# Performance work log

Measured on AMD Instinct MI355X. Metric: run time of the kernel, lower is better.

The kernel has to match this reference:

```python
import jax, jax.numpy as jnp
import numpy as np

EPS = 1e-7  # K.epsilon()


def setup_inputs() -> dict:
    key = jax.random.key(0)
    k1, k2, k3, k4 = jax.random.split(key, 4)
    B, T, S = 512, 32, 2048  # batch, time_steps, seq_len
    inputs = jax.random.normal(k1, (B, T, S), dtype=jnp.float32)
    # Keras mask (float 0/1), same shape as inputs
    mask = (jax.random.uniform(k2, (B, T, S)) < 0.8).astype(jnp.float32)
    # 'uniform' keras initializer: U(-0.05, 0.05)
    W = jax.random.uniform(k3, (S, T, T), minval=-0.05, maxval=0.05, dtype=jnp.float32)
    b = jax.random.uniform(k4, (S, T), minval=-0.05, maxval=0.05, dtype=jnp.float32)
    return {"inputs": inputs, "mask": mask, "W": W, "b": b}


def reference(inputs, mask, W, b):
    # (B,T,S) -> (B,S,T), apply mask
    x = jnp.transpose(inputs, (0, 2, 1)) * jnp.transpose(mask, (0, 2, 1))
    # per-position matmul, batched over B and S (replaces the tf.scan over batch)
    z = jnp.einsum('bst,stu->bsu', x, W) + b  # (B,S,T)
    e = jnp.exp(jnp.tanh(z))
    att = e / (jnp.sum(e, axis=2, keepdims=True) + EPS)  # softmax-like over T
    return jnp.sum(att * x, axis=1)  # (B,T)
```

## Files before the change

### kernel.cpp

```cpp
#include <hip/hip_runtime.h>

#define EPS_K 1e-7f

typedef __attribute__((ext_vector_type(8)))  short          frag8;
typedef __attribute__((ext_vector_type(16))) float          accf16;
typedef __attribute__((ext_vector_type(4)))  unsigned short us4;
typedef __attribute__((ext_vector_type(4)))  float          f32x4;

__device__ __forceinline__ unsigned f2bf(float f) {
  union { float f; unsigned u; } v; v.f = f;
  unsigned u = v.u;
  u += 0x7FFFu + ((u >> 16) & 1u);
  return u >> 16;
}
__device__ __forceinline__ float bf2f(unsigned short s) {
  union { unsigned u; float f; } v; v.u = ((unsigned)s) << 16;
  return v.f;
}
__device__ __forceinline__ unsigned pk_bf16(float lo, float hi) {
  return f2bf(lo) | (f2bf(hi) << 16);
}
__device__ __forceinline__ float rcp_f(float x) {
  return __builtin_amdgcn_rcpf(x);
}

__global__ __launch_bounds__(256) void wbf_prep(
    const float* __restrict__ Wt, unsigned short* __restrict__ Wbf)
{
  __shared__ unsigned short tile[32 * 33];
  const int s   = blockIdx.x;
  const int tid = threadIdx.x;
  {
    const int t  = tid >> 3;
    const int uc = tid & 7;
    const float4 v = *(const float4*)(Wt + s * 1024 + t * 32 + 4 * uc);
    tile[t * 33 + 4 * uc + 0] = (unsigned short)f2bf(v.x);
    tile[t * 33 + 4 * uc + 1] = (unsigned short)f2bf(v.y);
    tile[t * 33 + 4 * uc + 2] = (unsigned short)f2bf(v.z);
    tile[t * 33 + 4 * uc + 3] = (unsigned short)f2bf(v.w);
  }
  __syncthreads();
  {
    const int u  = tid >> 3;
    const int tc = tid & 7;
    uint2 d;
    d.x = (unsigned)tile[(4 * tc + 0) * 33 + u] | ((unsigned)tile[(4 * tc + 1) * 33 + u] << 16);
    d.y = (unsigned)tile[(4 * tc + 2) * 33 + u] | ((unsigned)tile[(4 * tc + 3) * 33 + u] << 16);
    *(uint2*)(Wbf + s * 1024 + u * 32 + 4 * tc) = d;
  }
}

__global__ __launch_bounds__(512, 2) void repack(
    const float* __restrict__ inp, const float* __restrict__ msk,
    unsigned short* __restrict__ Y)
{
  __shared__ unsigned short sl[32768];
  const int tid  = threadIdx.x;
  const int lane = tid & 63;
  const int b7   = tid >> 6;
  const int Q    = blockIdx.x & 63;
  const int w    = blockIdx.x >> 6;
  const int l31  = lane & 31;
  const int l5   = lane >> 5;

  const size_t rb = ((size_t)(Q * 8 + b7) * 32 + 8 * l5) * 2048 + w * 128 + 4 * l31;
  const int slot = b7 ^ (l31 & 7);

  #pragma unroll 1
  for (int c2 = 0; c2 < 2; ++c2) {
    f32x4 vi[8], vm[8];
    #pragma unroll
    for (int j = 0; j < 8; ++j) {
      const size_t off = rb + (size_t)(16 * c2 + j) * 2048;
      vi[j] = *(const f32x4*)(inp + off);
      vm[j] = *(const f32x4*)(msk + off);
    }
    const int c   = 2 * c2 + l5;
    const int sid = c * 8 + slot;
    #pragma unroll
    for (int k = 0; k < 4; ++k) {
      const int s_loc = 4 * l31 + k;
      uint4 d;
      d.x = pk_bf16(vi[0][k] * vm[0][k], vi[1][k] * vm[1][k]);
      d.y = pk_bf16(vi[2][k] * vm[2][k], vi[3][k] * vm[3][k]);
      d.z = pk_bf16(vi[4][k] * vm[4][k], vi[5][k] * vm[5][k]);
      d.w = pk_bf16(vi[6][k] * vm[6][k], vi[7][k] * vm[7][k]);
      *(uint4*)(sl + s_loc * 256 + ((sid ^ (s_loc & 7)) * 8)) = d;
    }
  }
  __syncthreads();

  const size_t ybyte = ((size_t)Q * 2048 + (size_t)w * 128) * 512;
  #pragma unroll
  for (int i = 0; i < 8; ++i) {
    const int e  = i * 512 + tid;
    const int sv = e >> 5, ch = e & 31;
    const uint4 d = *(const uint4*)(sl + sv * 256 + ((ch ^ (sv & 7)) * 8));
    *(uint4*)((char*)Y + ybyte + (size_t)e * 16) = d;
  }
}

__global__ __launch_bounds__(256, 4) void attn_comp(
    const unsigned short* __restrict__ Y,
    const unsigned short* __restrict__ Wbf,
    const float* __restrict__ bias,
    float* __restrict__ part)
{
  __shared__ float red[4096];
  const int tid  = threadIdx.x;
  const int bg   = blockIdx.x & 15;
  const int sg   = blockIdx.x >> 4;
  const int lane = tid & 63;
  const int wv   = tid >> 6;
  const int n    = lane & 31;
  const int h    = lane >> 5;

  const unsigned short* Yq = Y + ((size_t)(bg * 4 + (n >> 3)) * 2048) * 256;

  float O[16];
  #pragma unroll
  for (int r = 0; r < 16; ++r) O[r] = 0.f;

  #pragma unroll 2
  for (int it = 0; it < 8; ++it) {
    const int s = sg * 32 + wv * 8 + it;
    const unsigned short* slp = Yq + (size_t)s * 256;
    const int bt = (((n & 7) ^ ((s >> 2) & 7)) * 8);

    const frag8 b1 = *(const frag8*)(slp + h * 64 + bt);
    const frag8 b2 = *(const frag8*)(slp + (h + 2) * 64 + bt);

    const unsigned short* wp = Wbf + (size_t)s * 1024 + n * 32 + 8 * h;
    const frag8 a1 = *(const frag8*)(wp);
    const frag8 a2 = *(const frag8*)(wp + 16);

    accf16 acc;
    #pragma unroll
    for (int g = 0; g < 4; ++g) {
      const f32x4 bb = *(const f32x4*)(bias + s * 32 + 8 * g + 4 * h);
      acc[4 * g + 0] = bb[0]; acc[4 * g + 1] = bb[1];
      acc[4 * g + 2] = bb[2]; acc[4 * g + 3] = bb[3];
    }
    acc = __builtin_amdgcn_mfma_f32_32x32x16_bf16(a1, b1, acc, 0, 0, 0);
    acc = __builtin_amdgcn_mfma_f32_32x32x16_bf16(a2, b2, acc, 0, 0, 0);

    float ps = 0.f;
    #pragma unroll
    for (int r = 0; r < 16; ++r) {
      const float z  = acc[r];
      const float e2 = __expf(2.f * z);
      const float th = 1.f - 2.f * rcp_f(e2 + 1.f);
      acc[r] = __expf(th);
      ps    += acc[r];
    }
    const float tot = ps + __shfl_xor(ps, 32, 64);
    const float inv = rcp_f(tot + EPS_K);

    #pragma unroll
    for (int g = 0; g < 4; ++g) {
      const us4 xv = *(const us4*)(slp + g * 64 + bt + 4 * h);
      #pragma unroll
      for (int i = 0; i < 4; ++i)
        O[4 * g + i] += acc[4 * g + i] * inv * bf2f(xv[i]);
    }
  }

  #pragma unroll
  for (int r = 0; r < 16; ++r) {
    const int u = (r & 3) + 8 * (r >> 2) + 4 * h;
    red[wv * 1024 + n * 32 + (u ^ n)] = O[r];
  }
  __syncthreads();

  const int q0 = tid * 4;
  f32x4 v;
  #pragma unroll
  for (int i = 0; i < 4; ++i) {
    const int q = q0 + i;
    const int b = q >> 5, u = q & 31;
    float sum = 0.f;
    #pragma unroll
    for (int w = 0; w < 4; ++w) sum += red[w * 1024 + b * 32 + (u ^ b)];
    v[i] = sum;
  }
  *(f32x4*)(part + (size_t)sg * 16384 + bg * 1024 + q0) = v;
}

__global__ __launch_bounds__(256) void reduce_part(
    const float* __restrict__ part, float* __restrict__ out)
{
  const int f = blockIdx.x * 256 + threadIdx.x;
  float s = 0.f;
  #pragma unroll 8
  for (int sg = 0; sg < 64; ++sg) s += part[(size_t)sg * 16384 + f];
  out[f] = s;
}

__global__ __launch_bounds__(256) void attn_naive(
    const float* __restrict__ inp, const float* __restrict__ msk,
    const float* __restrict__ Wt, const float* __restrict__ bias,
    float* __restrict__ out)
{
  const int idx = blockIdx.x * 256 + threadIdx.x;
  const int b = idx >> 5, sc = idx & 31;
  float O[32];
  #pragma unroll
  for (int u = 0; u < 32; ++u) O[u] = 0.f;
  for (int si = 0; si < 64; ++si) {
    const int s = sc * 64 + si;
    float x[32], z[32];
    for (int t = 0; t < 32; ++t) {
      x[t] = inp[((size_t)b * 32 + t) * 2048 + s] * msk[((size_t)b * 32 + t) * 2048 + s];
      z[t] = bias[s * 32 + t];
    }
    for (int t = 0; t < 32; ++t) {
      const float xv = x[t];
      for (int u = 0; u < 32; ++u) z[u] += xv * Wt[(size_t)s * 1024 + t * 32 + u];
    }
    float e[32], ps = 0.f;
    for (int u = 0; u < 32; ++u) { e[u] = expf(tanhf(z[u])); ps += e[u]; }
    const float inv = 1.f / (ps + EPS_K);
    for (int u = 0; u < 32; ++u) O[u] += e[u] * inv * x[u];
  }
  for (int u = 0; u < 32; ++u) atomicAdd(out + b * 32 + u, O[u]);
}

extern "C" void kernel_launch(void* const* d_in, const int* in_sizes, int n_in,
                              void* d_out, int out_size, void* d_ws, size_t ws_size,
                              hipStream_t stream) {
  const float* inp  = (const float*)d_in[0];
  const float* msk  = (const float*)d_in[1];
  const float* Wt   = (const float*)d_in[2];
  const float* bias = (const float*)d_in[3];
  float* out = (float*)d_out;

  const size_t part_sz = (size_t)64 * 16384 * sizeof(float);
  const size_t wbf_sz  = (size_t)2048 * 1024 * sizeof(unsigned short);
  const size_t y_sz    = (size_t)512 * 32 * 2048 * sizeof(unsigned short);

  if (ws_size >= part_sz + wbf_sz + y_sz) {
    float* part = (float*)d_ws;
    unsigned short* Wbf = (unsigned short*)((char*)d_ws + part_sz);
    unsigned short* Y   = (unsigned short*)((char*)d_ws + part_sz + wbf_sz);
    repack<<<dim3(1024), dim3(512), 0, stream>>>(inp, msk, Y);
    wbf_prep<<<dim3(2048), dim3(256), 0, stream>>>(Wt, Wbf);
    attn_comp<<<dim3(1024), dim3(256), 0, stream>>>(Y, Wbf, bias, part);
    reduce_part<<<dim3(64), dim3(256), 0, stream>>>(part, out);
  } else {
    (void)hipMemsetAsync(out, 0, (size_t)out_size * sizeof(float), stream);
    attn_naive<<<dim3(64), dim3(256), 0, stream>>>(inp, msk, Wt, bias, out);
  }
}
```

Measured before the change: 347.8 us.

## Fuse masking and bf16 repack into attention kernel, dropping intermediate Y buffer

Removes the separate repack kernel that wrote a bf16 copy of the masked inputs to global memory. The attention kernel now loads inputs and mask with nontemporal loads, packs them into an LDS tile, and runs 16x16x32 MFMAs directly from shared memory. This saves a full write and re-read of the intermediate tensor and one launch, and halves the partial-sum buffer. In exchange each block needs 64KB of LDS, which limits occupancy, and the reads are exposed with no separate staging pass to hide them.

```diff
diff --git a/kernel.cpp b/kernel.cpp
--- a/kernel.cpp
+++ b/kernel.cpp
@@ -3,7 +3,7 @@
 #define EPS_K 1e-7f
 
 typedef __attribute__((ext_vector_type(8)))  short          frag8;
-typedef __attribute__((ext_vector_type(16))) float          accf16;
+typedef __attribute__((ext_vector_type(4)))  float          accf4;
 typedef __attribute__((ext_vector_type(4)))  unsigned short us4;
 typedef __attribute__((ext_vector_type(4)))  float          f32x4;
 
@@ -20,8 +20,8 @@
 __device__ __forceinline__ unsigned pk_bf16(float lo, float hi) {
   return f2bf(lo) | (f2bf(hi) << 16);
 }
-__device__ __forceinline__ float rcp_f(float x) {
-  return __builtin_amdgcn_rcpf(x);
+__device__ __forceinline__ f32x4 ld_nt(const float* p) {
+  return __builtin_nontemporal_load((const f32x4*)p);
 }
 
 __global__ __launch_bounds__(256) void wbf_prep(
@@ -50,140 +50,124 @@
   }
 }
 
-__global__ __launch_bounds__(512, 2) void repack(
-    const float* __restrict__ inp, const float* __restrict__ msk,
-    unsigned short* __restrict__ Y)
-{
-  __shared__ unsigned short sl[32768];
-  const int tid  = threadIdx.x;
-  const int lane = tid & 63;
-  const int b7   = tid >> 6;
-  const int Q    = blockIdx.x & 63;
-  const int w    = blockIdx.x >> 6;
-  const int l31  = lane & 31;
-  const int l5   = lane >> 5;
-
-  const size_t rb = ((size_t)(Q * 8 + b7) * 32 + 8 * l5) * 2048 + w * 128 + 4 * l31;
-  const int slot = b7 ^ (l31 & 7);
-
-  #pragma unroll 1
-  for (int c2 = 0; c2 < 2; ++c2) {
-    f32x4 vi[8], vm[8];
-    #pragma unroll
-    for (int j = 0; j < 8; ++j) {
-      const size_t off = rb + (size_t)(16 * c2 + j) * 2048;
-      vi[j] = *(const f32x4*)(inp + off);
-      vm[j] = *(const f32x4*)(msk + off);
-    }
-    const int c   = 2 * c2 + l5;
-    const int sid = c * 8 + slot;
-    #pragma unroll
-    for (int k = 0; k < 4; ++k) {
-      const int s_loc = 4 * l31 + k;
-      uint4 d;
-      d.x = pk_bf16(vi[0][k] * vm[0][k], vi[1][k] * vm[1][k]);
-      d.y = pk_bf16(vi[2][k] * vm[2][k], vi[3][k] * vm[3][k]);
-      d.z = pk_bf16(vi[4][k] * vm[4][k], vi[5][k] * vm[5][k]);
-      d.w = pk_bf16(vi[6][k] * vm[6][k], vi[7][k] * vm[7][k]);
-      *(uint4*)(sl + s_loc * 256 + ((sid ^ (s_loc & 7)) * 8)) = d;
-    }
-  }
-  __syncthreads();
-
-  const size_t ybyte = ((size_t)Q * 2048 + (size_t)w * 128) * 512;
-  #pragma unroll
-  for (int i = 0; i < 8; ++i) {
-    const int e  = i * 512 + tid;
-    const int sv = e >> 5, ch = e & 31;
-    const uint4 d = *(const uint4*)(sl + sv * 256 + ((ch ^ (sv & 7)) * 8));
-    *(uint4*)((char*)Y + ybyte + (size_t)e * 16) = d;
-  }
-}
-
-__global__ __launch_bounds__(256, 4) void attn_comp(
-    const unsigned short* __restrict__ Y,
+template <bool USE_WS>
+__global__ __launch_bounds__(512, 4) void attn_fused(
+    const float* __restrict__ inp,
+    const float* __restrict__ msk,
     const unsigned short* __restrict__ Wbf,
     const float* __restrict__ bias,
-    float* __restrict__ part)
-{
-  __shared__ float red[4096];
-  const int tid  = threadIdx.x;
-  const int bg   = blockIdx.x & 15;
-  const int sg   = blockIdx.x >> 4;
+    float* __restrict__ part,
+    float* __restrict__ out)
+{
+  __shared__ unsigned short x_us[16 * 2048];
+
+  const int tid = threadIdx.x;
+  const int st  = blockIdx.x & 31;
+  const int bg  = blockIdx.x >> 5;
+  const int s0  = st * 64;
+
+  const int sc = tid & 15;
+  const int bl = (tid >> 4) & 3;
+  const int hi = tid >> 6;
+  const int b_s = (hi & 3) * 4 + bl;
+  #pragma unroll
+  for (int it = 0; it < 2; ++it) {
+    const int tb = (hi >> 2) | (it << 1);
+    const float* ip = inp + ((size_t)(bg * 16 + b_s) * 32 + 8 * tb) * 2048 + s0 + 4 * sc;
+    const float* mp = msk + ((size_t)(bg * 16 + b_s) * 32 + 8 * tb) * 2048 + s0 + 4 * sc;
+    f32x4 vi[8], vm[8];
+    #pragma unroll
+    for (int r = 0; r < 8; ++r) {
+      vi[r] = ld_nt(ip + r * 2048);
+      vm[r] = ld_nt(mp + r * 2048);
+    }
+    #pragma unroll
+    for (int w = 0; w < 4; ++w) {
+      const int L = tb * 64 + 4 * sc + w;
+      uint4 d;
+      d.x = pk_bf16(vi[0][w] * vm[0][w], vi[1][w] * vm[1][w]);
+      d.y = pk_bf16(vi[2][w] * vm[2][w], vi[3][w] * vm[3][w]);
+      d.z = pk_bf16(vi[4][w] * vm[4][w], vi[5][w] * vm[5][w]);
+      d.w = pk_bf16(vi[6][w] * vm[6][w], vi[7][w] * vm[7][w]);
+      *(uint4*)(x_us + b_s * 2048 + ((L ^ (b_s & 7)) * 8)) = d;
+    }
+  }
+  __syncthreads();
+
   const int lane = tid & 63;
   const int wv   = tid >> 6;
-  const int n    = lane & 31;
-  const int h    = lane >> 5;
-
-  const unsigned short* Yq = Y + ((size_t)(bg * 4 + (n >> 3)) * 2048) * 256;
-
-  float O[16];
-  #pragma unroll
-  for (int r = 0; r < 16; ++r) O[r] = 0.f;
-
-  #pragma unroll 2
-  for (int it = 0; it < 8; ++it) {
-    const int s = sg * 32 + wv * 8 + it;
-    const unsigned short* slp = Yq + (size_t)s * 256;
-    const int bt = (((n & 7) ^ ((s >> 2) & 7)) * 8);
-
-    const frag8 b1 = *(const frag8*)(slp + h * 64 + bt);
-    const frag8 b2 = *(const frag8*)(slp + (h + 2) * 64 + bt);
-
-    const unsigned short* wp = Wbf + (size_t)s * 1024 + n * 32 + 8 * h;
-    const frag8 a1 = *(const frag8*)(wp);
-    const frag8 a2 = *(const frag8*)(wp + 16);
-
-    accf16 acc;
-    #pragma unroll
-    for (int g = 0; g < 4; ++g) {
-      const f32x4 bb = *(const f32x4*)(bias + s * 32 + 8 * g + 4 * h);
-      acc[4 * g + 0] = bb[0]; acc[4 * g + 1] = bb[1];
-      acc[4 * g + 2] = bb[2]; acc[4 * g + 3] = bb[3];
-    }
-    acc = __builtin_amdgcn_mfma_f32_32x32x16_bf16(a1, b1, acc, 0, 0, 0);
-    acc = __builtin_amdgcn_mfma_f32_32x32x16_bf16(a2, b2, acc, 0, 0, 0);
-
+  const int n16  = lane & 15;
+  const int kg   = lane >> 4;
+  const int nx   = n16 & 7;
+  const int kg2  = kg >> 1, kw = kg & 1;
+
+  float O1[4], O2[4];
+  #pragma unroll
+  for (int i = 0; i < 4; ++i) { O1[i] = 0.f; O2[i] = 0.f; }
+
+  #pragma unroll
+  for (int si = 0; si < 8; ++si) {
+    const int sl = wv * 8 + si;
+    const int s  = s0 + sl;
+
+    const frag8 a1 = *(const frag8*)(Wbf + (size_t)s * 1024 + n16 * 32 + kg * 8);
+    const frag8 a2 = *(const frag8*)(Wbf + (size_t)s * 1024 + (16 + n16) * 32 + kg * 8);
+    const frag8 bf = *(const frag8*)(x_us + n16 * 2048 + (((kg * 64 + sl) ^ nx) * 8));
+
+    accf4 acc1, acc2;
+    {
+      const f32x4 bb1 = *(const f32x4*)(bias + s * 32 + kg * 4);
+      const f32x4 bb2 = *(const f32x4*)(bias + s * 32 + 16 + kg * 4);
+      acc1[0] = bb1[0]; acc1[1] = bb1[1]; acc1[2] = bb1[2]; acc1[3] = bb1[3];
+      acc2[0] = bb2[0]; acc2[1] = bb2[1]; acc2[2] = bb2[2]; acc2[3] = bb2[3];
+    }
+    acc1 = __builtin_amdgcn_mfma_f32_16x16x32_bf16(a1, bf, acc1, 0, 0, 0);
+    acc2 = __builtin_amdgcn_mfma_f32_16x16x32_bf16(a2, bf, acc2, 0, 0, 0);
+
+    float e1[4], e2[4];
     float ps = 0.f;
     #pragma unroll
-    for (int r = 0; r < 16; ++r) {
-      const float z  = acc[r];
-      const float e2 = __expf(2.f * z);
-      const float th = 1.f - 2.f * rcp_f(e2 + 1.f);
-      acc[r] = __expf(th);
-      ps    += acc[r];
-    }
-    const float tot = ps + __shfl_xor(ps, 32, 64);
-    const float inv = rcp_f(tot + EPS_K);
-
-    #pragma unroll
-    for (int g = 0; g < 4; ++g) {
-      const us4 xv = *(const us4*)(slp + g * 64 + bt + 4 * h);
-      #pragma unroll
-      for (int i = 0; i < 4; ++i)
-        O[4 * g + i] += acc[4 * g + i] * inv * bf2f(xv[i]);
-    }
-  }
-
-  #pragma unroll
-  for (int r = 0; r < 16; ++r) {
-    const int u = (r & 3) + 8 * (r >> 2) + 4 * h;
-    red[wv * 1024 + n * 32 + (u ^ n)] = O[r];
-  }
-  __syncthreads();
-
-  const int q0 = tid * 4;
-  f32x4 v;
+    for (int i = 0; i < 4; ++i) {
+      const float za = acc1[i], zb = acc2[i];
+      const float ea = __expf(2.f * za), eb = __expf(2.f * zb);
+      e1[i] = __expf(1.f - 2.f / (ea + 1.f));
+      e2[i] = __expf(1.f - 2.f / (eb + 1.f));
+      ps += e1[i] + e2[i];
+    }
+    float t1  = ps + __shfl_xor(ps, 16, 64);
+    const float tot = t1 + __shfl_xor(t1, 32, 64);
+    const float inv = 1.f / (tot + EPS_K);
+
+    const us4 xv1 = *(const us4*)(x_us + n16 * 2048 + (((kg2 * 64 + sl) ^ nx) * 8) + 4 * kw);
+    const us4 xv2 = *(const us4*)(x_us + n16 * 2048 + ((((2 + kg2) * 64 + sl) ^ nx) * 8) + 4 * kw);
+    #pragma unroll
+    for (int i = 0; i < 4; ++i) {
+      O1[i] += e1[i] * inv * bf2f(xv1[i]);
+      O2[i] += e2[i] * inv * bf2f(xv2[i]);
+    }
+  }
+
+  __syncthreads();
+  float* red = (float*)x_us;
   #pragma unroll
   for (int i = 0; i < 4; ++i) {
-    const int q = q0 + i;
-    const int b = q >> 5, u = q & 31;
-    float sum = 0.f;
-    #pragma unroll
-    for (int w = 0; w < 4; ++w) sum += red[w * 1024 + b * 32 + (u ^ b)];
-    v[i] = sum;
-  }
-  *(f32x4*)(part + (size_t)sg * 16384 + bg * 1024 + q0) = v;
+    const int u1 = kg * 4 + i;
+    const int u2 = 16 + kg * 4 + i;
+    red[wv * 512 + n16 * 32 + (u1 ^ n16)] = O1[i];
+    red[wv * 512 + n16 * 32 + (u2 ^ n16)] = O2[i];
+  }
+  __syncthreads();
+
+  const int q  = tid;
+  const int bq = q >> 5, uq = q & 31;
+  float sum = 0.f;
+  #pragma unroll
+  for (int w = 0; w < 8; ++w) sum += red[w * 512 + bq * 32 + (uq ^ bq)];
+  if (USE_WS) {
+    part[(size_t)st * 16384 + bg * 512 + q] = sum;
+  } else {
+    atomicAdd(out + bg * 512 + q, sum);
+  }
 }
 
 __global__ __launch_bounds__(256) void reduce_part(
@@ -192,7 +176,7 @@
   const int f = blockIdx.x * 256 + threadIdx.x;
   float s = 0.f;
   #pragma unroll 8
-  for (int sg = 0; sg < 64; ++sg) s += part[(size_t)sg * 16384 + f];
+  for (int st = 0; st < 32; ++st) s += part[(size_t)st * 16384 + f];
   out[f] = s;
 }
 
@@ -234,18 +218,22 @@
   const float* bias = (const float*)d_in[3];
   float* out = (float*)d_out;
 
-  const size_t part_sz = (size_t)64 * 16384 * sizeof(float);
+  const size_t part_sz = (size_t)32 * 16384 * sizeof(float);
   const size_t wbf_sz  = (size_t)2048 * 1024 * sizeof(unsigned short);
-  const size_t y_sz    = (size_t)512 * 32 * 2048 * sizeof(unsigned short);
-
-  if (ws_size >= part_sz + wbf_sz + y_sz) {
+
+  if (ws_size >= part_sz + wbf_sz) {
     float* part = (float*)d_ws;
     unsigned short* Wbf = (unsigned short*)((char*)d_ws + part_sz);
-    unsigned short* Y   = (unsigned short*)((char*)d_ws + part_sz + wbf_sz);
-    repack<<<dim3(1024), dim3(512), 0, stream>>>(inp, msk, Y);
     wbf_prep<<<dim3(2048), dim3(256), 0, stream>>>(Wt, Wbf);
-    attn_comp<<<dim3(1024), dim3(256), 0, stream>>>(Y, Wbf, bias, part);
+    attn_fused<true><<<dim3(1024), dim3(512), 0, stream>>>(
+        inp, msk, Wbf, bias, part, out);
     reduce_part<<<dim3(64), dim3(256), 0, stream>>>(part, out);
+  } else if (ws_size >= wbf_sz) {
+    unsigned short* Wbf = (unsigned short*)d_ws;
+    (void)hipMemsetAsync(out, 0, (size_t)out_size * sizeof(float), stream);
+    wbf_prep<<<dim3(2048), dim3(256), 0, stream>>>(Wt, Wbf);
+    attn_fused<false><<<dim3(1024), dim3(512), 0, stream>>>(
+        inp, msk, Wbf, bias, nullptr, out);
   } else {
     (void)hipMemsetAsync(out, 0, (size_t)out_size * sizeof(float), stream);
     attn_naive<<<dim3(64), dim3(256), 0, stream>>>(inp, msk, Wt, bias, out);
```

Result: faster. 279.9 us (-19.5%).
